# Kernel optimization log

Measured on AMD Instinct MI355X. Metric: run time of the kernel, lower is better.

## Reference

```python
import jax, jax.numpy as jnp
import numpy as np

EPS_BN = 1e-5
K_DET = 50

def conv2d(x, w, b, pad):
    y = jax.lax.conv_general_dilated(x, w, (1, 1), [(pad, pad), (pad, pad)],
                                     dimension_numbers=('NCHW', 'OIHW', 'NCHW'))
    return y + b[None, :, None, None]

def branch2(x, w1, b1, w2, b2):
    # conv3x3 -> relu -> conv1x1
    return conv2d(jax.nn.relu(conv2d(x, w1, b1, 1)), w2, b2, 0)

def roi_head(x, w1, b1, g, beta, m, v, w2, b2):
    # conv3x3 -> BN(eval) -> relu -> global avg pool -> conv1x1
    h = conv2d(x, w1, b1, 1)
    h = (h - m[None, :, None, None]) * (g[None, :, None, None] / jnp.sqrt(v[None, :, None, None] + EPS_BN)) + beta[None, :, None, None]
    h = jax.nn.relu(h)
    h = jnp.mean(h, axis=(2, 3), keepdims=True)
    return conv2d(h, w2, b2, 0)[:, :, 0, 0]

def nms_hm(heat, kernel=3):
    pad = (kernel - 1) // 2
    hmax = jax.lax.reduce_window(heat, -jnp.inf, jax.lax.max,
                                 (1, 1, kernel, kernel), (1, 1, 1, 1),
                                 [(0, 0), (0, 0), (pad, pad), (pad, pad)])
    return heat * (hmax == heat).astype(heat.dtype)

def select_topk(heat, K):
    B, C, H, W = heat.shape
    s_all, i_all = jax.lax.top_k(heat.reshape(B, C, H * W), K)   # per-class topk
    scores, idx = jax.lax.top_k(s_all.reshape(B, C * K), K)      # overall topk
    classes = idx // K
    inds = jnp.take_along_axis(i_all.reshape(B, C * K), idx, axis=1)  # flat HW inds
    return scores, inds, classes

def roi_align_7x7(feat, boxes, sr=2):
    # torchvision roi_align, spatial_scale=1, aligned=False, sampling_ratio=sr
    B, C, H, W = feat.shape
    N = boxes.shape[0]
    b = boxes[:, 0].astype(jnp.int32)
    x1, y1, x2, y2 = boxes[:, 1], boxes[:, 2], boxes[:, 3], boxes[:, 4]
    roi_w = jnp.maximum(x2 - x1, 1.0)
    roi_h = jnp.maximum(y2 - y1, 1.0)
    bw = roi_w / 7.0
    bh = roi_h / 7.0
    S = 7 * sr
    off = (jnp.arange(S, dtype=feat.dtype) + 0.5) / sr  # sample offsets in bin units
    xs = x1[:, None] + bw[:, None] * off[None, :]       # (N,S)
    ys = y1[:, None] + bh[:, None] * off[None, :]
    X = jnp.broadcast_to(xs[:, None, :], (N, S, S))
    Y = jnp.broadcast_to(ys[:, :, None], (N, S, S))
    valid = (X > -1.0) & (X < W) & (Y > -1.0) & (Y < H)
    Xc = jnp.clip(X, 0.0, W - 1.0)
    Yc = jnp.clip(Y, 0.0, H - 1.0)
    x0 = jnp.floor(Xc).astype(jnp.int32)
    y0 = jnp.floor(Yc).astype(jnp.int32)
    x1i = jnp.minimum(x0 + 1, W - 1)
    y1i = jnp.minimum(y0 + 1, H - 1)
    lx = Xc - x0
    ly = Yc - y0
    flat = feat.transpose(0, 2, 3, 1).reshape(B * H * W, C)
    base = (b * H * W)[:, None, None]
    g = lambda yy, xx: flat[base + yy * W + xx]  # (N,S,S,C)
    v = (((1 - ly) * (1 - lx))[..., None] * g(y0, x0)
         + ((1 - ly) * lx)[..., None] * g(y0, x1i)
         + (ly * (1 - lx))[..., None] * g(y1i, x0)
         + (ly * lx)[..., None] * g(y1i, x1i))
    v = v * valid[..., None]
    v = v.reshape(N, 7, sr, 7, sr, C).mean(axis=(2, 4))
    return v.transpose(0, 3, 1, 2)  # (N,C,7,7)

def project_to_rect(calib, pts):
    c_u, c_v = calib[:, 0, 2], calib[:, 1, 2]
    f_u, f_v = calib[:, 0, 0], calib[:, 1, 1]
    b_x = calib[:, 0, 3] / (-f_u)
    b_y = calib[:, 1, 3] / (-f_v)
    x = (pts[:, 0] - c_u) * pts[:, 2] / f_u + b_x
    y = (pts[:, 1] - c_v) * pts[:, 2] / f_v + b_y
    return jnp.stack([x, y, pts[:, 2]], -1)

HEAD_NAMES = ['dep', 'o3', 's3', 'hd']

def setup_inputs():
    key = jax.random.key(0)
    ks = iter(jax.random.split(key, 64))
    B, Cin, H, W = 8, 64, 96, 320
    HC, NC = 256, 3
    f32 = jnp.float32
    rn = lambda shape, s=0.02: s * jax.random.normal(next(ks), shape, f32)
    inp = {}
    inp['features'] = jax.random.normal(next(ks), (B, Cin, H, W), f32)
    base = jnp.array([[700., 0., 640., 0.], [0., 700., 192., 0.], [0., 0., 1., 0.]], f32)
    inp['calib'] = base[None] + (jax.random.uniform(next(ks), (B, 3, 4), f32) - 0.5) * 2.0
    crb = jnp.array([[0., 0.], [1280., 384.]], f32)
    inp['coord_ranges'] = crb[None] + (jax.random.uniform(next(ks), (B, 2, 2), f32) - 0.5) * 2.0
    inp['mean_size'] = jnp.array([[3.88, 1.63, 1.53], [0.84, 0.66, 1.76], [1.76, 0.60, 1.73]], f32)
    inp['hm_w1'] = rn((HC, Cin, 3, 3)); inp['hm_b1'] = jnp.zeros(HC, f32)
    inp['hm_w2'] = rn((3, HC, 1, 1)); inp['hm_b2'] = jnp.full((3,), -np.log(1 / 0.1 - 1), f32)
    inp['o2_w1'] = rn((HC, Cin, 3, 3)); inp['o2_b1'] = jnp.zeros(HC, f32)
    inp['o2_w2'] = rn((2, HC, 1, 1)); inp['o2_b2'] = jnp.zeros(2, f32)
    inp['s2_w1'] = rn((HC, Cin, 3, 3)); inp['s2_b1'] = jnp.zeros(HC, f32)
    inp['s2_w2'] = rn((2, HC, 1, 1)); inp['s2_b2'] = 8.0 * jnp.ones(2, f32)
    Croi = Cin + 2 + NC
    for name, oc in zip(HEAD_NAMES, [2, 2, 4, 24]):
        inp[name + '_w1'] = rn((HC, Croi, 3, 3)); inp[name + '_b1'] = jnp.zeros(HC, f32)
        inp[name + '_g'] = 1.0 + 0.1 * jax.random.normal(next(ks), (HC,), f32)
        inp[name + '_beta'] = 0.1 * jax.random.normal(next(ks), (HC,), f32)
        inp[name + '_m'] = 0.1 * jax.random.normal(next(ks), (HC,), f32)
        inp[name + '_v'] = 1.0 + jax.random.uniform(next(ks), (HC,), f32)
        inp[name + '_w2'] = rn((oc, HC, 1, 1)); inp[name + '_b2'] = jnp.zeros(oc, f32)
    return inp

def reference(features, calib, coord_ranges, mean_size,
              hm_w1, hm_b1, hm_w2, hm_b2,
              o2_w1, o2_b1, o2_w2, o2_b2,
              s2_w1, s2_b1, s2_w2, s2_b2,
              dep_w1, dep_b1, dep_g, dep_beta, dep_m, dep_v, dep_w2, dep_b2,
              o3_w1, o3_b1, o3_g, o3_beta, o3_m, o3_v, o3_w2, o3_b2,
              s3_w1, s3_b1, s3_g, s3_beta, s3_m, s3_v, s3_w2, s3_b2,
              hd_w1, hd_b1, hd_g, hd_beta, hd_m, hd_v, hd_w2, hd_b2):
    B, Cf, H, W = features.shape
    dt = features.dtype
    heatmap = branch2(features, hm_w1, hm_b1, hm_w2, hm_b2)    # (B,3,H,W)
    offset_2d = branch2(features, o2_w1, o2_b1, o2_w2, o2_b2)  # (B,2,H,W)
    size_2d = branch2(features, s2_w1, s2_b1, s2_w2, s2_b2)    # (B,2,H,W)
    heat = nms_hm(heatmap)
    _, inds, classes = select_topk(heat, K_DET)                # (B,K)
    # coord map and box2d maps (B,5,H,W): [batch_idx, x1,y1,x2,y2]
    xs = jnp.arange(W, dtype=dt)
    ys = jnp.arange(H, dtype=dt)
    coord = jnp.stack([jnp.broadcast_to(xs[None, :], (H, W)),
                       jnp.broadcast_to(ys[:, None], (H, W))], 0)[None]
    center = coord + offset_2d
    bidx = jnp.broadcast_to(jnp.arange(B, dtype=dt)[:, None, None, None], (B, 1, H, W))
    box2d_maps = jnp.concatenate([bidx, center - size_2d / 2, center + size_2d / 2], 1)
    bm = box2d_maps.reshape(B, 5, H * W).transpose(0, 2, 1)    # (B,HW,5)
    boxes = jnp.take_along_axis(bm, inds[:, :, None], axis=1).reshape(-1, 5)  # (N,5)
    N = boxes.shape[0]
    roi_feat = roi_align_7x7(features, boxes)                  # (N,C,7,7)
    rb = boxes[:, 0].astype(jnp.int32)
    cr = coord_ranges[rb]                                      # (N,2,2)
    sx = cr[:, 1, 0] - cr[:, 0, 0]
    sy = cr[:, 1, 1] - cr[:, 0, 1]
    box_img = jnp.stack([boxes[:, 0],
                         boxes[:, 1] / W * sx + cr[:, 0, 0],
                         boxes[:, 2] / H * sy + cr[:, 0, 1],
                         boxes[:, 3] / W * sx + cr[:, 0, 0],
                         boxes[:, 4] / H * sy + cr[:, 0, 1]], -1)
    roi_calib = calib[rb]                                      # (N,3,4)
    ones = jnp.ones((N, 1), dt)
    p1 = project_to_rect(roi_calib, jnp.concatenate([box_img[:, 1:3], ones], -1))[:, :2]
    p2 = project_to_rect(roi_calib, jnp.concatenate([box_img[:, 3:5], ones], -1))[:, :2]
    t = jnp.arange(7, dtype=dt) / 6.0
    cx = p1[:, 0:1] + t[None, :] * (p2[:, 0:1] - p1[:, 0:1])   # (N,7)
    cy = p1[:, 1:2] + t[None, :] * (p2[:, 1:2] - p1[:, 1:2])
    coord_maps = jnp.stack([jnp.broadcast_to(cx[:, None, :], (N, 7, 7)),
                            jnp.broadcast_to(cy[:, :, None], (N, 7, 7))], 1)
    cls = classes.reshape(-1)
    NC = mean_size.shape[0]
    cls_hot = jax.nn.one_hot(cls, NC, dtype=dt)
    roi_in = jnp.concatenate([roi_feat, coord_maps,
                              jnp.broadcast_to(cls_hot[:, :, None, None], (N, NC, 7, 7))], 1)
    box2d_h = jnp.maximum(box_img[:, 4] - box_img[:, 2], 1.0)
    s3 = roi_head(roi_in, s3_w1, s3_b1, s3_g, s3_beta, s3_m, s3_v, s3_w2, s3_b2)  # (N,4)
    h3d_log_std = s3[:, 3:4]
    size3d_offset = s3[:, :3]
    size_3d = mean_size[cls] + size3d_offset
    f_u = roi_calib[:, 0, 0]
    depth_geo = size_3d[:, 0] / box2d_h * f_u
    dep = roi_head(roi_in, dep_w1, dep_b1, dep_g, dep_beta, dep_m, dep_v, dep_w2, dep_b2)
    depth_geo_log_std = (h3d_log_std[:, 0] + 2.0 * (jnp.log(f_u) - jnp.log(box2d_h)))[:, None]
    depth_log_std = jax.nn.logsumexp(jnp.concatenate([dep[:, 1:2], depth_geo_log_std], -1), axis=-1, keepdims=True)
    depth = jnp.concatenate([1.0 / (jax.nn.sigmoid(dep[:, 0:1]) + 1e-6) - 1.0 + depth_geo[:, None],
                             depth_log_std], -1)
    heading = roi_head(roi_in, hd_w1, hd_b1, hd_g, hd_beta, hd_m, hd_v, hd_w2, hd_b2)
    offset_3d = roi_head(roi_in, o3_w1, o3_b1, o3_g, o3_beta, o3_m, o3_v, o3_w2, o3_b2)
    return (heatmap, offset_2d, size_2d, heading, depth, offset_3d, size3d_offset, h3d_log_std)
```

## Files before the change

kernel.cpp:

```cpp
#include <hip/hip_runtime.h>
#include <math.h>

typedef unsigned short u16;
typedef unsigned int   u32;
typedef unsigned long long u64;
typedef __attribute__((ext_vector_type(8))) short short8;
typedef __attribute__((ext_vector_type(4))) float f32x4;

__device__ __forceinline__ float b2f(u16 v) { return __uint_as_float(((u32)v) << 16); }
__device__ __forceinline__ u16 f2b(float f) {
    u32 u = __float_as_uint(f);
    u32 r = (u + 0x7FFFu + ((u >> 16) & 1u)) >> 16;
    return (u16)r;
}
__device__ __forceinline__ float gload(const void* p, long i, int bf) {
    return bf ? b2f(((const u16*)p)[i]) : ((const float*)p)[i];
}
__device__ __forceinline__ void gstore(void* p, long i, float v, int bf) {
    if (bf) ((u16*)p)[i] = f2b(v);
    else    ((float*)p)[i] = v;
}

__device__ __forceinline__ u64 packKey(float v, int idx) {
    u32 u = __float_as_uint(v);
    u32 m = (u & 0x80000000u) ? ~u : (u | 0x80000000u);
    return ((u64)(~m) << 32) | (u32)idx;
}

#define BATCH 8
#define CIN   64
#define FH    96
#define FW    320
#define KDET  50
#define NROI  400
#define CROI  69
#define HW    (FH*FW)
#define CHUNK 1920
#define NCHUNK 16

#define WS_HEAT 0L
#define WS_OFF2 737280L
#define WS_SIZ2 1228800L
#define WS_NH   1720320L
#define WS_S1S  2457600L
#define WS_S1I  2458800L
#define WS_CLS  2460000L
#define WS_BOX  2460400L
#define WS_ROI  2462400L
#define WS_HOUT 3814800L
#define WS_W1T  3827600L
#define WS_WB16 3975056L
#define WS_W1H  4269968L
#define WS_PAR  4905872L
#define WS_FLAG 4938960L

#define PB_CAL 0
#define PB_CRN 96
#define PB_MSZ 128
#define PB_BR0 144
#define PB_HD0 3264

#define O_HEAT 0L
#define O_OFF2 737280L
#define O_SIZ2 1228800L
#define O_HEAD 1720320L
#define O_DEP  1729920L
#define O_OFF3 1730720L
#define O_S3D  1731520L
#define O_H3D  1732720L

__global__ void kDetect(const void* __restrict__ feat, int* __restrict__ flag) {
    __shared__ int cnt;
    if (threadIdx.x == 0) cnt = 0;
    __syncthreads();
    u16 v = ((const u16*)feat)[threadIdx.x];
    float f = b2f(v);
    u32 e = (v >> 7) & 0xFF;
    float a = fabsf(f);
    int sane = (e != 0xFF) && (f == 0.f || (a >= 1e-8f && a <= 1e4f));
    atomicAdd(&cnt, sane);
    __syncthreads();
    if (threadIdx.x == 0) *flag = (cnt >= 480) ? 1 : 0;
}

struct WPtrs { const void* bw[3]; const void* hw[4]; };

__global__ void kPrepW(WPtrs P, const int* __restrict__ flag,
                       float* __restrict__ w1t, u16* __restrict__ wb16,
                       u16* __restrict__ whb) {
    const int bf = *flag;
    int idx = blockIdx.x * 256 + threadIdx.x;
    if (idx < 147456) {
        int k = idx >> 8, c = idx & 255;
        w1t[idx] = gload(P.bw[0], (long)c * 576 + k, bf);
    } else if (idx < 589824) {
        int j = idx - 147456;
        int br = j / 147456, rem = j % 147456;
        int tap = rem / 16384;
        int r2 = rem & 16383;
        int s = r2 >> 13;
        int n = (r2 >> 5) & 255;
        int c5 = r2 & 31;
        int ci = s * 32 + c5;
        wb16[j] = f2b(gload(P.bw[br], (long)n * 576 + ci * 9 + tap, bf));
    } else {
        int j = idx - 589824;
        int h = j / 221184, rem = j % 221184;
        int tap = rem / 24576, rem2 = rem % 24576;
        int cs = rem2 / 8192, rem3 = rem2 % 8192;
        int oc = rem3 >> 5, jj = rem3 & 31;
        int ci = cs * 32 + jj;
        u16 val = 0;
        if (ci < CROI) val = f2b(gload(P.hw[h], (long)oc * 621 + ci * 9 + tap, bf));
        whb[j] = val;
    }
}

struct Seg { const void* src; int n; int dst; };
struct Segs { Seg s[40]; };

__global__ void kPrepP(Segs S, const int* __restrict__ flag, float* __restrict__ par) {
    const int bf = *flag;
    Seg sg = S.s[blockIdx.x];
    for (int i = threadIdx.x; i < sg.n; i += 256)
        par[sg.dst + i] = gload(sg.src, i, bf);
}

union B3U {
    u16   a[4][68][72];
    float red[8][64][3];
};

__global__ __launch_bounds__(512, 4)
void kBranch3(const void* __restrict__ feat, const int* __restrict__ flag,
              const u16* __restrict__ wbAll,
              const float* __restrict__ bpAll,
              void* __restrict__ outb, float* __restrict__ wsbase) {
    __shared__ __align__(16) B3U u;

    const long obase[3] = {O_HEAT, O_OFF2, O_SIZ2};
    const long wfs[3]   = {WS_HEAT, WS_OFF2, WS_SIZ2};

    const int bfl = *flag;
    const int tid = threadIdx.x;
    const int wave = tid >> 6, lane = tid & 63;
    const int q = lane >> 4, n15 = lane & 15;
    const int mg = wave >> 2, ng = wave & 3;
    const int x0 = blockIdx.x * 64, y0 = blockIdx.y * 2;
    const int br = blockIdx.z >> 3, b = blockIdx.z & 7;
    const int oc = (br == 0) ? 3 : 2;
    const u16* wpt = wbAll + br * 147456;
    const float* bp = bpAll + br * 1040;

    if (tid < 256) {
        const int ci = tid & 63, rr = tid >> 6;
        const int gy = y0 - 1 + rr;
        if (gy < 0 || gy >= FH) {
            for (int xi = 0; xi < 66; ++xi) u.a[rr][xi][ci] = 0;
        } else if (bfl) {
            const u16* rp = (const u16*)feat + ((long)((b << 6) | ci) * FH + gy) * FW;
            for (int j = 0; j < 10; ++j) {
                int xs0 = x0 - 8 + j * 8;
                u16 tmp[8];
                if (xs0 >= 0 && xs0 <= FW - 8)
                    *(uint4*)tmp = *(const uint4*)(rp + xs0);
                else
                    for (int e = 0; e < 8; ++e) {
                        int gx = xs0 + e;
                        tmp[e] = (gx >= 0 && gx < FW) ? rp[gx] : (u16)0;
                    }
                for (int e = 0; e < 8; ++e) {
                    int xi = xs0 + e - x0 + 1;
                    if (xi >= 0 && xi < 66) u.a[rr][xi][ci] = tmp[e];
                }
            }
        } else {
            const float* rp = (const float*)feat + ((long)((b << 6) | ci) * FH + gy) * FW;
            for (int j = 0; j < 18; ++j) {
                int xs0 = x0 - 4 + j * 4;
                float tmp[4];
                if (xs0 >= 0 && xs0 <= FW - 4)
                    *(float4*)tmp = *(const float4*)(rp + xs0);
                else
                    for (int e = 0; e < 4; ++e) {
                        int gx = xs0 + e;
                        tmp[e] = (gx >= 0 && gx < FW) ? rp[gx] : 0.f;
                    }
                for (int e = 0; e < 4; ++e) {
                    int xi = xs0 + e - x0 + 1;
                    if (xi >= 0 && xi < 66) u.a[rr][xi][ci] = f2b(tmp[e]);
                }
            }
        }
    }
    __syncthreads();

    f32x4 acc[4][4];
#pragma unroll
    for (int i = 0; i < 4; ++i)
#pragma unroll
        for (int t = 0; t < 4; ++t) acc[i][t] = (f32x4){0.f, 0.f, 0.f, 0.f};

#pragma unroll 1
    for (int tap = 0; tap < 9; ++tap) {
        const int ky = tap / 3, kx = tap % 3;
#pragma unroll
        for (int s = 0; s < 2; ++s) {
            const u16* wks = wpt + (tap * 2 + s) * 8192;
            short8 bfr[4];
#pragma unroll
            for (int t = 0; t < 4; ++t)
                bfr[t] = *(const short8*)(wks + (ng * 64 + t * 16 + n15) * 32 + q * 8);
            short8 afr[4];
#pragma unroll
            for (int i = 0; i < 4; ++i)
                afr[i] = *(const short8*)&u.a[mg + ky][i * 16 + n15 + kx][s * 32 + q * 8];
#pragma unroll
            for (int i = 0; i < 4; ++i)
#pragma unroll
                for (int t = 0; t < 4; ++t)
                    acc[i][t] = __builtin_amdgcn_mfma_f32_16x16x32_bf16(
                        afr[i], bfr[t], acc[i][t], 0, 0, 0);
        }
    }

    float b1v[4], w2v[3][4];
#pragma unroll
    for (int t = 0; t < 4; ++t) {
        int n = ng * 64 + t * 16 + n15;
        b1v[t] = bp[n];
#pragma unroll
        for (int k = 0; k < 3; ++k) w2v[k][t] = bp[256 + k * 256 + n];
    }
    __syncthreads();
#pragma unroll
    for (int i = 0; i < 4; ++i) {
#pragma unroll
        for (int r = 0; r < 4; ++r) {
            float pk[3];
#pragma unroll
            for (int k = 0; k < 3; ++k) pk[k] = 0.f;
#pragma unroll
            for (int t = 0; t < 4; ++t) {
                float h = fmaxf(acc[i][t][r] + b1v[t], 0.f);
#pragma unroll
                for (int k = 0; k < 3; ++k) pk[k] = fmaf(h, w2v[k][t], pk[k]);
            }
#pragma unroll
            for (int k = 0; k < 3; ++k) {
                pk[k] += __shfl_xor(pk[k], 1);
                pk[k] += __shfl_xor(pk[k], 2);
                pk[k] += __shfl_xor(pk[k], 4);
                pk[k] += __shfl_xor(pk[k], 8);
            }
            if (n15 == 0) {
                int ml = i * 16 + q * 4 + r;
#pragma unroll
                for (int k = 0; k < 3; ++k) u.red[wave][ml][k] = pk[k];
            }
        }
    }
    __syncthreads();
    float* outf = wsbase + wfs[br];
    for (int t2 = tid; t2 < oc * 128; t2 += 512) {
        int k = t2 >> 7, m = t2 & 127;
        int row = m >> 6, x = m & 63;
        int mg2 = m >> 6, ml = m & 63;
        float s = bp[256 + oc * 256 + k];
#pragma unroll
        for (int w = 0; w < 4; ++w) s += u.red[mg2 * 4 + w][ml][k];
        long o = (((long)b * oc + k) * FH + (y0 + row)) * FW + x0 + x;
        gstore(outb, obase[br] + o, s, bfl);
        outf[o] = s;
    }
}

union BrLds {
    float w[36 * 256];
    float part[32 * 3 * 32];
};

__global__ __launch_bounds__(256)
void kBranchX(const void* __restrict__ feat, const int* __restrict__ flag,
              const float* __restrict__ w1t, const float* __restrict__ bp,
              void* __restrict__ outb, long obase, float* __restrict__ outf) {
    __shared__ float in_lds[4][3][36];
    __shared__ BrLds u;
    const int bf = *flag;
    const int OC = 3;

    const int tid = threadIdx.x;
    const int xg = tid & 7, cg = tid >> 3;
    const int x0 = blockIdx.x * 32, y = blockIdx.y, b = blockIdx.z;
    const int c0 = cg * 8;

    float acc[8][4];
#pragma unroll
    for (int i = 0; i < 8; ++i)
#pragma unroll
        for (int j = 0; j < 4; ++j) acc[i][j] = 0.f;

    for (int chunk = 0; chunk < 16; ++chunk) {
        const int ci0 = chunk * 4;
        __syncthreads();
        for (int i = tid; i < 4 * 3 * 36; i += 256) {
            int xx = i % 36, t2 = i / 36;
            int r = t2 % 3, ci = t2 / 3;
            int gx = x0 - 1 + xx, gy = y - 1 + r;
            float v = 0.f;
            if (gx >= 0 && gx < FW && gy >= 0 && gy < FH)
                v = gload(feat, ((long)(b * CIN + ci0 + ci) * FH + gy) * FW + gx, bf);
            in_lds[ci][r][xx] = v;
        }
        {
            const float4* src = (const float4*)(w1t + (long)ci0 * 9 * 256);
            float4* dst = (float4*)u.w;
            for (int i = tid; i < 36 * 256 / 4; i += 256) dst[i] = src[i];
        }
        __syncthreads();
#pragma unroll
        for (int ci = 0; ci < 4; ++ci) {
#pragma unroll
            for (int ky = 0; ky < 3; ++ky) {
                const float* rowp = &in_lds[ci][ky][xg * 4];
                float inv[6];
                *(float4*)&inv[0] = *(const float4*)&rowp[0];
                *(float2*)&inv[4] = *(const float2*)&rowp[4];
#pragma unroll
                for (int kx = 0; kx < 3; ++kx) {
                    const float* wp = &u.w[(ci * 9 + ky * 3 + kx) * 256 + c0];
                    float wv[8];
                    *(float4*)&wv[0] = *(const float4*)&wp[0];
                    *(float4*)&wv[4] = *(const float4*)&wp[4];
#pragma unroll
                    for (int cc = 0; cc < 8; ++cc)
#pragma unroll
                        for (int xx = 0; xx < 4; ++xx)
                            acc[cc][xx] = fmaf(wv[cc], inv[xx + kx], acc[cc][xx]);
                }
            }
        }
    }

#pragma unroll
    for (int cc = 0; cc < 8; ++cc) {
        float b1v = bp[c0 + cc];
#pragma unroll
        for (int xx = 0; xx < 4; ++xx)
            acc[cc][xx] = fmaxf(acc[cc][xx] + b1v, 0.f);
    }

    __syncthreads();
#pragma unroll
    for (int k = 0; k < OC; ++k) {
        float p[4];
#pragma unroll
        for (int xx = 0; xx < 4; ++xx) p[xx] = 0.f;
#pragma unroll
        for (int cc = 0; cc < 8; ++cc) {
            float wv = bp[256 + k * 256 + c0 + cc];
#pragma unroll
            for (int xx = 0; xx < 4; ++xx) p[xx] = fmaf(acc[cc][xx], wv, p[xx]);
        }
#pragma unroll
        for (int xx = 0; xx < 4; ++xx)
            u.part[(cg * OC + k) * 32 + xg * 4 + xx] = p[xx];
    }
    __syncthreads();
    for (int t = tid; t < OC * 32; t += 256) {
        int k = t >> 5, xx = t & 31;
        float s = bp[256 + OC * 256 + k];
#pragma unroll 8
        for (int g = 0; g < 32; ++g) s += u.part[(g * OC + k) * 32 + xx];
        long o = (((long)b * OC + k) * FH + y) * FW + x0 + xx;
        gstore(outb, obase + o, s, bf);
        outf[o] = s;
    }
}

__global__ void kNms(const float* __restrict__ heat, float* __restrict__ nh) {
    int idx = blockIdx.x * 256 + threadIdx.x;
    if (idx >= 737280) return;
    int x = idx % FW, t = idx / FW;
    int yy = t % FH, bc = t / FH;
    const float* p = heat + (long)bc * HW;
    float v = p[yy * FW + x];
    float m = v;
    for (int dy = -1; dy <= 1; ++dy) {
        int ny = yy + dy;
        if (ny < 0 || ny >= FH) continue;
        for (int dx = -1; dx <= 1; ++dx) {
            int nx = x + dx;
            if (nx < 0 || nx >= FW) continue;
            m = fmaxf(m, p[ny * FW + nx]);
        }
    }
    nh[idx] = (v == m) ? v : 0.f;
}

__global__ __launch_bounds__(256)
void kTopA(float* __restrict__ nh) {
    __shared__ u64 keys[CHUNK];
    const int bc = blockIdx.x, ch = blockIdx.y;
    const int tid = threadIdx.x;
    const long base = (long)bc * HW + (long)ch * CHUNK;
    for (int i = tid; i < CHUNK; i += 256)
        keys[i] = packKey(nh[base + i], ch * CHUNK + i);
    __syncthreads();
    if (tid < 64) {
        const int lane = tid;
        u64* outp = (u64*)(nh + base);
        for (int it = 0; it < KDET; ++it) {
            u64 bk = ~0ULL; int bp = 0;
            for (int i = lane; i < CHUNK; i += 64) {
                u64 k = keys[i];
                if (k < bk) { bk = k; bp = i; }
            }
#pragma unroll
            for (int s = 32; s > 0; s >>= 1) {
                u64 k2 = __shfl_down(bk, s);
                int p2 = __shfl_down(bp, s);
                if (k2 < bk) { bk = k2; bp = p2; }
            }
            bk = __shfl(bk, 0);
            bp = __shfl(bp, 0);
            if (lane == 0) {
                outp[it] = bk;
                keys[bp] = ~0ULL;
            }
        }
    }
}

__global__ __launch_bounds__(64)
void kTopB(const float* __restrict__ nh, float* __restrict__ s1s,
           int* __restrict__ s1i) {
    __shared__ u64 keys[NCHUNK * KDET];
    const int bc = blockIdx.x, lane = threadIdx.x;
    for (int ch = 0; ch < NCHUNK; ++ch) {
        const u64* src = (const u64*)(nh + (long)bc * HW + (long)ch * CHUNK);
        if (lane < KDET) keys[ch * KDET + lane] = src[lane];
    }
    __syncthreads();
    for (int it = 0; it < KDET; ++it) {
        u64 bk = ~0ULL; int bp = 0;
        for (int i = lane; i < NCHUNK * KDET; i += 64) {
            u64 k = keys[i];
            if (k < bk) { bk = k; bp = i; }
        }
#pragma unroll
        for (int s = 32; s > 0; s >>= 1) {
            u64 k2 = __shfl_down(bk, s);
            int p2 = __shfl_down(bp, s);
            if (k2 < bk) { bk = k2; bp = p2; }
        }
        bk = __shfl(bk, 0);
        bp = __shfl(bp, 0);
        if (lane == 0) {
            u32 hm = ~(u32)(bk >> 32);
            u32 u = (hm & 0x80000000u) ? (hm & 0x7fffffffu) : ~hm;
            s1s[bc * KDET + it] = __uint_as_float(u);
            s1i[bc * KDET + it] = (int)(bk & 0xFFFFFFFFu);
            keys[bp] = ~0ULL;
        }
    }
}

__global__ void kTop2(const float* __restrict__ s1s, const int* __restrict__ s1i,
                      const float* __restrict__ off2, const float* __restrict__ siz2,
                      float* __restrict__ boxes, int* __restrict__ clsArr) {
    const int b = blockIdx.x, t = threadIdx.x;
    __shared__ float sc[150];
    for (int i = t; i < 150; i += 64) sc[i] = s1s[b * 150 + i];
    __syncthreads();
    for (int r = 0; r < KDET; ++r) {
        float bv = -INFINITY; int bp = 0x7fffffff;
        for (int i = t; i < 150; i += 64) {
            float v = sc[i];
            if (v > bv) { bv = v; bp = i; }
        }
        for (int s = 32; s > 0; s >>= 1) {
            float v2 = __shfl_down(bv, s);
            int   p2 = __shfl_down(bp, s);
            if (v2 > bv || (v2 == bv && p2 < bp)) { bv = v2; bp = p2; }
        }
        if (t == 0) {
            int cls = bp / KDET;
            int ind = s1i[b * 150 + bp];
            int n = b * KDET + r;
            clsArr[n] = cls;
            int x = ind % FW, yy = ind / FW;
            float cx = (float)x  + off2[(((long)b * 2 + 0) * FH + yy) * FW + x];
            float cy = (float)yy + off2[(((long)b * 2 + 1) * FH + yy) * FW + x];
            float w  = siz2[(((long)b * 2 + 0) * FH + yy) * FW + x];
            float h  = siz2[(((long)b * 2 + 1) * FH + yy) * FW + x];
            boxes[n * 5 + 0] = (float)b;
            boxes[n * 5 + 1] = cx - w * 0.5f;
            boxes[n * 5 + 2] = cy - h * 0.5f;
            boxes[n * 5 + 3] = cx + w * 0.5f;
            boxes[n * 5 + 4] = cy + h * 0.5f;
            sc[bp] = -INFINITY;
        }
        __syncthreads();
    }
}

__global__ __launch_bounds__(256)
void kRoi(const void* __restrict__ feat, const int* __restrict__ flag,
          const float* __restrict__ boxes, const int* __restrict__ clsArr,
          const float* __restrict__ par, float* __restrict__ roi_in) {
    const int n = blockIdx.x, tid = threadIdx.x;
    const int bf = *flag;
    __shared__ int   x0s[14], x1s[14], y0s[14], y1s[14], vxs[14], vys[14];
    __shared__ float lxs[14], lys[14], cxs[7], cys[7];

    const float bx1 = boxes[n * 5 + 1], by1 = boxes[n * 5 + 2];
    const float bx2 = boxes[n * 5 + 3], by2 = boxes[n * 5 + 4];
    const int b = (int)boxes[n * 5 + 0];

    if (tid < 14) {
        float roi_w = fmaxf(bx2 - bx1, 1.f);
        float X = bx1 + (roi_w / 7.f) * ((tid + 0.5f) * 0.5f);
        vxs[tid] = (X > -1.f) && (X < (float)FW);
        float Xc = fminf(fmaxf(X, 0.f), (float)(FW - 1));
        int xi = (int)floorf(Xc);
        x0s[tid] = xi; x1s[tid] = min(xi + 1, FW - 1); lxs[tid] = Xc - (float)xi;
    } else if (tid >= 16 && tid < 30) {
        int i = tid - 16;
        float roi_h = fmaxf(by2 - by1, 1.f);
        float Y = by1 + (roi_h / 7.f) * ((i + 0.5f) * 0.5f);
        vys[i] = (Y > -1.f) && (Y < (float)FH);
        float Yc = fminf(fmaxf(Y, 0.f), (float)(FH - 1));
        int yi = (int)floorf(Yc);
        y0s[i] = yi; y1s[i] = min(yi + 1, FH - 1); lys[i] = Yc - (float)yi;
    } else if (tid >= 32 && tid < 46) {
        int j = tid - 32;
        const float* cal = par + PB_CAL + b * 12;
        float f_u = cal[0], c_u = cal[2], t03 = cal[3];
        float f_v = cal[5], c_v = cal[6], t13 = cal[7];
        float bxc = t03 / (-f_u), byc = t13 / (-f_v);
        const float* cr = par + PB_CRN + b * 4;
        float crx0 = cr[0], cry0 = cr[1], crx1 = cr[2], cry1 = cr[3];
        float sx = crx1 - crx0, sy = cry1 - cry0;
        float u1 = bx1 / (float)FW * sx + crx0, v1 = by1 / (float)FH * sy + cry0;
        float u2 = bx2 / (float)FW * sx + crx0, v2 = by2 / (float)FH * sy + cry0;
        float p1x = (u1 - c_u) / f_u + bxc, p1y = (v1 - c_v) / f_v + byc;
        float p2x = (u2 - c_u) / f_u + bxc, p2y = (v2 - c_v) / f_v + byc;
        if (j < 7) cxs[j] = p1x + ((float)j / 6.f) * (p2x - p1x);
        else       cys[j - 7] = p1y + ((float)(j - 7) / 6.f) * (p2y - p1y);
    }
    __syncthreads();

    for (int t = tid; t < CIN * 49; t += 256) {
        int c = t / 49, p = t % 49, oy = p / 7, ox = p % 7;
        long fb = ((long)b * CIN + c) * HW;
        float acc = 0.f;
#pragma unroll
        for (int dy = 0; dy < 2; ++dy) {
            int sy = oy * 2 + dy;
            float ly = lys[sy]; int yA = y0s[sy], yB = y1s[sy], vy = vys[sy];
#pragma unroll
            for (int dx = 0; dx < 2; ++dx) {
                int sx = ox * 2 + dx;
                float lx = lxs[sx]; int xA = x0s[sx], xB = x1s[sx];
                float v = (1.f - ly) * (1.f - lx) * gload(feat, fb + yA * FW + xA, bf)
                        + (1.f - ly) * lx         * gload(feat, fb + yA * FW + xB, bf)
                        + ly * (1.f - lx)         * gload(feat, fb + yB * FW + xA, bf)
                        + ly * lx                 * gload(feat, fb + yB * FW + xB, bf);
                if (!(vy && vxs[sx])) v = 0.f;
                acc += v;
            }
        }
        roi_in[((long)n * CROI + c) * 49 + p] = acc * 0.25f;
    }
    int cls = clsArr[n];
    for (int t = tid; t < 5 * 49; t += 256) {
        int ch = t / 49, p = t % 49, i = p / 7, j = p % 7;
        float v;
        if (ch == 0)      v = cxs[j];
        else if (ch == 1) v = cys[i];
        else              v = (cls == ch - 2) ? 1.f : 0.f;
        roi_in[((long)n * CROI + 64 + ch) * 49 + p] = v;
    }
}

__global__ __launch_bounds__(256, 4)
void kHeadM(const float* __restrict__ roi_in, const u16* __restrict__ whb,
            const float* __restrict__ par, float* __restrict__ head_out) {
    const int h = blockIdx.x, n = blockIdx.y, tid = threadIdx.x;
    const int wave = tid >> 6, lane = tid & 63;
    const int q = lane >> 4, n15 = lane & 15;
    const int ocArr[4] = {2, 2, 4, 24};
    const int offArr[4] = {0, 2, 4, 8};
    __shared__ __align__(16) u16 r_lds[9][9][104];
    __shared__ float means[256];

    for (int i = tid; i < 9 * 9 * 104 / 8; i += 256)
        ((uint4*)r_lds)[i] = (uint4){0, 0, 0, 0};
    __syncthreads();
    const float* rp = roi_in + (long)n * CROI * 49;
    for (int i = tid; i < CROI * 49; i += 256) {
        int c = i / 49, p = i % 49;
        r_lds[p / 7 + 1][p % 7 + 1][c] = f2b(rp[i]);
    }
    __syncthreads();

    int oyA[4], oxA[4];
#pragma unroll
    for (int i = 0; i < 4; ++i) {
        int pos = i * 16 + n15; if (pos > 48) pos = 48;
        oyA[i] = pos / 7; oxA[i] = pos % 7;
    }

    f32x4 acc[4][4];
#pragma unroll
    for (int i = 0; i < 4; ++i)
#pragma unroll
        for (int t = 0; t < 4; ++t) acc[i][t] = (f32x4){0.f, 0.f, 0.f, 0.f};

#pragma unroll 1
    for (int tap = 0; tap < 9; ++tap) {
        const int ky = tap / 3, kx = tap % 3;
        const u16* wt = whb + ((long)h * 9 + tap) * 24576;
#pragma unroll
        for (int cs = 0; cs < 3; ++cs) {
            short8 afr[4], bfr[4];
#pragma unroll
            for (int i = 0; i < 4; ++i)
                afr[i] = *(const short8*)&r_lds[oyA[i] + ky][oxA[i] + kx][cs * 32 + q * 8];
#pragma unroll
            for (int t = 0; t < 4; ++t)
                bfr[t] = *(const short8*)(wt + ((cs << 8) + wave * 64 + t * 16 + n15) * 32 + q * 8);
#pragma unroll
            for (int i = 0; i < 4; ++i)
#pragma unroll
                for (int t = 0; t < 4; ++t)
                    acc[i][t] = __builtin_amdgcn_mfma_f32_16x16x32_bf16(
                        afr[i], bfr[t], acc[i][t], 0, 0, 0);
        }
    }

    const float* hb = par + PB_HD0 + h * 7456;
#pragma unroll
    for (int t = 0; t < 4; ++t) {
        int oc = wave * 64 + t * 16 + n15;
        float b1 = hb[oc], g = hb[256 + oc], be = hb[512 + oc];
        float m = hb[768 + oc], v = hb[1024 + oc];
        float scale = g / sqrtf(v + 1e-5f);
        float s = 0.f;
#pragma unroll
        for (int i = 0; i < 4; ++i)
#pragma unroll
            for (int r = 0; r < 4; ++r) {
                int pos = i * 16 + q * 4 + r;
                if (pos < 49)
                    s += fmaxf((acc[i][t][r] + b1 - m) * scale + be, 0.f);
            }
        s += __shfl_xor(s, 16);
        s += __shfl_xor(s, 32);
        if (q == 0) means[oc] = s / 49.f;
    }
    __syncthreads();

    int oc_out = ocArr[h];
    const float* w2 = hb + 1280;
    for (int k = wave; k < oc_out; k += 4) {
        float s = 0.f;
        for (int c = lane; c < 256; c += 64) s += means[c] * w2[k * 256 + c];
#pragma unroll
        for (int off = 32; off > 0; off >>= 1) s += __shfl_down(s, off);
        if (lane == 0)
            head_out[(long)n * 32 + offArr[h] + k] = s + w2[oc_out * 256 + k];
    }
}

__global__ void kFinal(const float* __restrict__ head_out, const float* __restrict__ boxes,
                       const int* __restrict__ clsArr, const float* __restrict__ par,
                       void* __restrict__ out, const int* __restrict__ flag) {
    int n = blockIdx.x * 256 + threadIdx.x;
    if (n >= NROI) return;
    const int bf = *flag;
    const float* ho = head_out + (long)n * 32;
    float dep0 = ho[0], dep1 = ho[1];
    int b = (int)boxes[n * 5 + 0];
    int cls = clsArr[n];

    for (int j = 0; j < 24; ++j) gstore(out, O_HEAD + n * 24 + j, ho[8 + j], bf);
    gstore(out, O_OFF3 + n * 2 + 0, ho[2], bf);
    gstore(out, O_OFF3 + n * 2 + 1, ho[3], bf);
    gstore(out, O_S3D + n * 3 + 0, ho[4], bf);
    gstore(out, O_S3D + n * 3 + 1, ho[5], bf);
    gstore(out, O_S3D + n * 3 + 2, ho[6], bf);
    gstore(out, O_H3D + n, ho[7], bf);

    float cry0 = par[PB_CRN + b * 4 + 1], cry1 = par[PB_CRN + b * 4 + 3];
    float sy = cry1 - cry0;
    float bi2 = boxes[n * 5 + 2] / (float)FH * sy + cry0;
    float bi4 = boxes[n * 5 + 4] / (float)FH * sy + cry0;
    float box_h = fmaxf(bi4 - bi2, 1.f);
    float f_u = par[PB_CAL + b * 12 + 0];
    float size3d0 = par[PB_MSZ + cls * 3 + 0] + ho[4];
    float depth_geo = size3d0 / box_h * f_u;
    float sig = 1.f / (1.f + expf(-dep0));
    float d0 = 1.f / (sig + 1e-6f) - 1.f + depth_geo;
    float dgls = ho[7] + 2.f * (logf(f_u) - logf(box_h));
    float mx = fmaxf(dep1, dgls);
    float lse = mx + logf(expf(dep1 - mx) + expf(dgls - mx));
    gstore(out, O_DEP + n * 2 + 0, d0, bf);
    gstore(out, O_DEP + n * 2 + 1, lse, bf);
}

extern "C" void kernel_launch(void* const* d_in, const int* in_sizes, int n_in,
                              void* d_out, int out_size, void* d_ws, size_t ws_size,
                              hipStream_t stream) {
    (void)in_sizes; (void)n_in; (void)out_size; (void)ws_size;
    float* ws = (float*)d_ws;
    float* par = ws + WS_PAR;
    int* flag = (int*)(ws + WS_FLAG);
    u16* wb16 = (u16*)(ws + WS_WB16);
    u16* whb  = (u16*)(ws + WS_W1H);
    const void* feat = d_in[0];

    kDetect<<<1, 512, 0, stream>>>(feat, flag);

    WPtrs WP;
    WP.bw[0] = d_in[4]; WP.bw[1] = d_in[8]; WP.bw[2] = d_in[12];
    WP.hw[0] = d_in[16]; WP.hw[1] = d_in[24]; WP.hw[2] = d_in[32]; WP.hw[3] = d_in[40];
    kPrepW<<<5760, 256, 0, stream>>>(WP, flag, ws + WS_W1T, wb16, whb);

    Segs SG; int si = 0;
    auto add = [&](const void* s, int n, int dst) {
        SG.s[si].src = s; SG.s[si].n = n; SG.s[si].dst = dst; ++si;
    };
    add(d_in[1], 96, PB_CAL); add(d_in[2], 32, PB_CRN); add(d_in[3], 9, PB_MSZ);
    const int ocb[3] = {3, 2, 2};
    for (int b = 0; b < 3; ++b) {
        int base = PB_BR0 + b * 1040;
        int i0 = 4 + 4 * b;
        add(d_in[i0 + 1], 256, base);
        add(d_in[i0 + 2], ocb[b] * 256, base + 256);
        add(d_in[i0 + 3], ocb[b], base + 256 + ocb[b] * 256);
    }
    const int och[4] = {2, 2, 4, 24};
    for (int h = 0; h < 4; ++h) {
        int base = PB_HD0 + h * 7456;
        int i0 = 16 + 8 * h;
        add(d_in[i0 + 1], 256, base);
        add(d_in[i0 + 2], 256, base + 256);
        add(d_in[i0 + 3], 256, base + 512);
        add(d_in[i0 + 4], 256, base + 768);
        add(d_in[i0 + 5], 256, base + 1024);
        add(d_in[i0 + 6], och[h] * 256, base + 1280);
        add(d_in[i0 + 7], och[h], base + 1280 + och[h] * 256);
    }
    kPrepP<<<si, 256, 0, stream>>>(SG, flag, par);

    kBranch3<<<dim3(5, 48, 24), 512, 0, stream>>>(
        feat, flag, wb16, par + PB_BR0, d_out, ws);

    kBranchX<<<dim3(10, 3, 8), 256, 0, stream>>>(
        feat, flag, ws + WS_W1T, par + PB_BR0, d_out, O_HEAT, ws + WS_HEAT);

    kNms<<<2880, 256, 0, stream>>>(ws + WS_HEAT, ws + WS_NH);
    kTopA<<<dim3(24, NCHUNK), 256, 0, stream>>>(ws + WS_NH);
    kTopB<<<24, 64, 0, stream>>>(ws + WS_NH, ws + WS_S1S, (int*)(ws + WS_S1I));
    kTop2<<<8, 64, 0, stream>>>(ws + WS_S1S, (int*)(ws + WS_S1I), ws + WS_OFF2,
                                ws + WS_SIZ2, ws + WS_BOX, (int*)(ws + WS_CLS));
    kRoi<<<400, 256, 0, stream>>>(feat, flag, ws + WS_BOX, (int*)(ws + WS_CLS),
                                  par, ws + WS_ROI);
    kHeadM<<<dim3(4, NROI), 256, 0, stream>>>(ws + WS_ROI, whb, par, ws + WS_HOUT);
    kFinal<<<2, 256, 0, stream>>>(ws + WS_HOUT, ws + WS_BOX, (int*)(ws + WS_CLS),
                                  par, d_out, flag);
}
```

Measured before the change: 914.2 us.

## Fuse prep, NMS+topk stages and loop branches inside kBranch3

Merges the dtype detection, weight prep and parameter prep kernels into one launch, with every block recomputing the bf16/fp32 flag locally. Fuses the 3x3 heatmap NMS into the per-chunk top-k kernel using an LDS row tile, and merges the per-class and overall top-k stages into one kernel. kBranch3 now loops over the three branches inside each block so the staged input tile is loaded once rather than three times. This removes several launches and intermediate round trips, but the branch kernel has a third as many blocks and does three times the work per block.

```diff
diff --git a/kernel.cpp b/kernel.cpp
--- a/kernel.cpp
+++ b/kernel.cpp
@@ -25,6 +25,23 @@
     u32 u = __float_as_uint(v);
     u32 m = (u & 0x80000000u) ? ~u : (u | 0x80000000u);
     return ((u64)(~m) << 32) | (u32)idx;
+}
+
+__device__ int blockFlag(const void* feat) {
+    __shared__ int fcnt;
+    if (threadIdx.x == 0) fcnt = 0;
+    __syncthreads();
+    int sane = 0;
+    for (int i = threadIdx.x; i < 512; i += blockDim.x) {
+        u16 v = ((const u16*)feat)[i];
+        float f = b2f(v);
+        u32 e = (v >> 7) & 0xFF;
+        float a = fabsf(f);
+        sane += (e != 0xFF) && (f == 0.f || (a >= 1e-8f && a <= 1e4f));
+    }
+    atomicAdd(&fcnt, sane);
+    __syncthreads();
+    return fcnt >= 480;
 }
 
 #define BATCH 8
@@ -69,74 +86,59 @@
 #define O_S3D  1731520L
 #define O_H3D  1732720L
 
-__global__ void kDetect(const void* __restrict__ feat, int* __restrict__ flag) {
-    __shared__ int cnt;
-    if (threadIdx.x == 0) cnt = 0;
-    __syncthreads();
-    u16 v = ((const u16*)feat)[threadIdx.x];
-    float f = b2f(v);
-    u32 e = (v >> 7) & 0xFF;
-    float a = fabsf(f);
-    int sane = (e != 0xFF) && (f == 0.f || (a >= 1e-8f && a <= 1e4f));
-    atomicAdd(&cnt, sane);
-    __syncthreads();
-    if (threadIdx.x == 0) *flag = (cnt >= 480) ? 1 : 0;
-}
-
 struct WPtrs { const void* bw[3]; const void* hw[4]; };
-
-__global__ void kPrepW(WPtrs P, const int* __restrict__ flag,
-                       float* __restrict__ w1t, u16* __restrict__ wb16,
-                       u16* __restrict__ whb) {
-    const int bf = *flag;
-    int idx = blockIdx.x * 256 + threadIdx.x;
-    if (idx < 147456) {
-        int k = idx >> 8, c = idx & 255;
-        w1t[idx] = gload(P.bw[0], (long)c * 576 + k, bf);
-    } else if (idx < 589824) {
-        int j = idx - 147456;
-        int br = j / 147456, rem = j % 147456;
-        int tap = rem / 16384;
-        int r2 = rem & 16383;
-        int s = r2 >> 13;
-        int n = (r2 >> 5) & 255;
-        int c5 = r2 & 31;
-        int ci = s * 32 + c5;
-        wb16[j] = f2b(gload(P.bw[br], (long)n * 576 + ci * 9 + tap, bf));
+struct Seg { const void* src; int n; int dst; };
+struct Segs { Seg s[40]; int cnt; };
+
+__global__ void kPrepWP(WPtrs P, Segs S, const void* __restrict__ feat,
+                        int* __restrict__ flag, float* __restrict__ w1t,
+                        u16* __restrict__ wb16, u16* __restrict__ whb,
+                        float* __restrict__ par) {
+    const int bf = blockFlag(feat);
+    if (blockIdx.x == 0 && threadIdx.x == 0) *flag = bf;
+    if (blockIdx.x < 5760) {
+        int idx = blockIdx.x * 256 + threadIdx.x;
+        if (idx < 147456) {
+            int k = idx >> 8, c = idx & 255;
+            w1t[idx] = gload(P.bw[0], (long)c * 576 + k, bf);
+        } else if (idx < 589824) {
+            int j = idx - 147456;
+            int br = j / 147456, rem = j % 147456;
+            int tap = rem / 16384;
+            int r2 = rem & 16383;
+            int s = r2 >> 13;
+            int n = (r2 >> 5) & 255;
+            int c5 = r2 & 31;
+            int ci = s * 32 + c5;
+            wb16[j] = f2b(gload(P.bw[br], (long)n * 576 + ci * 9 + tap, bf));
+        } else {
+            int j = idx - 589824;
+            int h = j / 221184, rem = j % 221184;
+            int tap = rem / 24576, rem2 = rem % 24576;
+            int cs = rem2 / 8192, rem3 = rem2 % 8192;
+            int oc = rem3 >> 5, jj = rem3 & 31;
+            int ci = cs * 32 + jj;
+            u16 val = 0;
+            if (ci < CROI) val = f2b(gload(P.hw[h], (long)oc * 621 + ci * 9 + tap, bf));
+            whb[j] = val;
+        }
     } else {
-        int j = idx - 589824;
-        int h = j / 221184, rem = j % 221184;
-        int tap = rem / 24576, rem2 = rem % 24576;
-        int cs = rem2 / 8192, rem3 = rem2 % 8192;
-        int oc = rem3 >> 5, jj = rem3 & 31;
-        int ci = cs * 32 + jj;
-        u16 val = 0;
-        if (ci < CROI) val = f2b(gload(P.hw[h], (long)oc * 621 + ci * 9 + tap, bf));
-        whb[j] = val;
-    }
-}
-
-struct Seg { const void* src; int n; int dst; };
-struct Segs { Seg s[40]; };
-
-__global__ void kPrepP(Segs S, const int* __restrict__ flag, float* __restrict__ par) {
-    const int bf = *flag;
-    Seg sg = S.s[blockIdx.x];
-    for (int i = threadIdx.x; i < sg.n; i += 256)
-        par[sg.dst + i] = gload(sg.src, i, bf);
-}
-
-union B3U {
-    u16   a[4][68][72];
-    float red[8][64][3];
-};
+        int sidx = blockIdx.x - 5760;
+        if (sidx < S.cnt) {
+            Seg sg = S.s[sidx];
+            for (int i = threadIdx.x; i < sg.n; i += 256)
+                par[sg.dst + i] = gload(sg.src, i, bf);
+        }
+    }
+}
 
 __global__ __launch_bounds__(512, 4)
 void kBranch3(const void* __restrict__ feat, const int* __restrict__ flag,
               const u16* __restrict__ wbAll,
               const float* __restrict__ bpAll,
               void* __restrict__ outb, float* __restrict__ wsbase) {
-    __shared__ __align__(16) B3U u;
+    __shared__ __align__(16) u16 a_lds[4][68][72];
+    __shared__ float red[8][64][3];
 
     const long obase[3] = {O_HEAT, O_OFF2, O_SIZ2};
     const long wfs[3]   = {WS_HEAT, WS_OFF2, WS_SIZ2};
@@ -147,16 +149,13 @@
     const int q = lane >> 4, n15 = lane & 15;
     const int mg = wave >> 2, ng = wave & 3;
     const int x0 = blockIdx.x * 64, y0 = blockIdx.y * 2;
-    const int br = blockIdx.z >> 3, b = blockIdx.z & 7;
-    const int oc = (br == 0) ? 3 : 2;
-    const u16* wpt = wbAll + br * 147456;
-    const float* bp = bpAll + br * 1040;
+    const int b = blockIdx.z;
 
     if (tid < 256) {
         const int ci = tid & 63, rr = tid >> 6;
         const int gy = y0 - 1 + rr;
         if (gy < 0 || gy >= FH) {
-            for (int xi = 0; xi < 66; ++xi) u.a[rr][xi][ci] = 0;
+            for (int xi = 0; xi < 66; ++xi) a_lds[rr][xi][ci] = 0;
         } else if (bfl) {
             const u16* rp = (const u16*)feat + ((long)((b << 6) | ci) * FH + gy) * FW;
             for (int j = 0; j < 10; ++j) {
@@ -171,7 +170,7 @@
                     }
                 for (int e = 0; e < 8; ++e) {
                     int xi = xs0 + e - x0 + 1;
-                    if (xi >= 0 && xi < 66) u.a[rr][xi][ci] = tmp[e];
+                    if (xi >= 0 && xi < 66) a_lds[rr][xi][ci] = tmp[e];
                 }
             }
         } else {
@@ -188,90 +187,97 @@
                     }
                 for (int e = 0; e < 4; ++e) {
                     int xi = xs0 + e - x0 + 1;
-                    if (xi >= 0 && xi < 66) u.a[rr][xi][ci] = f2b(tmp[e]);
+                    if (xi >= 0 && xi < 66) a_lds[rr][xi][ci] = f2b(tmp[e]);
                 }
             }
         }
     }
     __syncthreads();
 
-    f32x4 acc[4][4];
-#pragma unroll
-    for (int i = 0; i < 4; ++i)
-#pragma unroll
-        for (int t = 0; t < 4; ++t) acc[i][t] = (f32x4){0.f, 0.f, 0.f, 0.f};
-
 #pragma unroll 1
-    for (int tap = 0; tap < 9; ++tap) {
-        const int ky = tap / 3, kx = tap % 3;
-#pragma unroll
-        for (int s = 0; s < 2; ++s) {
-            const u16* wks = wpt + (tap * 2 + s) * 8192;
-            short8 bfr[4];
-#pragma unroll
-            for (int t = 0; t < 4; ++t)
-                bfr[t] = *(const short8*)(wks + (ng * 64 + t * 16 + n15) * 32 + q * 8);
-            short8 afr[4];
-#pragma unroll
-            for (int i = 0; i < 4; ++i)
-                afr[i] = *(const short8*)&u.a[mg + ky][i * 16 + n15 + kx][s * 32 + q * 8];
-#pragma unroll
-            for (int i = 0; i < 4; ++i)
+    for (int br = 0; br < 3; ++br) {
+        const int oc = (br == 0) ? 3 : 2;
+        const u16* wpt = wbAll + br * 147456;
+        const float* bp = bpAll + br * 1040;
+
+        f32x4 acc[4][4];
+#pragma unroll
+        for (int i = 0; i < 4; ++i)
+#pragma unroll
+            for (int t = 0; t < 4; ++t) acc[i][t] = (f32x4){0.f, 0.f, 0.f, 0.f};
+
+#pragma unroll 1
+        for (int tap = 0; tap < 9; ++tap) {
+            const int ky = tap / 3, kx = tap % 3;
+#pragma unroll
+            for (int s = 0; s < 2; ++s) {
+                const u16* wks = wpt + (tap * 2 + s) * 8192;
+                short8 bfr[4];
 #pragma unroll
                 for (int t = 0; t < 4; ++t)
-                    acc[i][t] = __builtin_amdgcn_mfma_f32_16x16x32_bf16(
-                        afr[i], bfr[t], acc[i][t], 0, 0, 0);
-        }
-    }
-
-    float b1v[4], w2v[3][4];
-#pragma unroll
-    for (int t = 0; t < 4; ++t) {
-        int n = ng * 64 + t * 16 + n15;
-        b1v[t] = bp[n];
-#pragma unroll
-        for (int k = 0; k < 3; ++k) w2v[k][t] = bp[256 + k * 256 + n];
-    }
-    __syncthreads();
-#pragma unroll
-    for (int i = 0; i < 4; ++i) {
-#pragma unroll
-        for (int r = 0; r < 4; ++r) {
-            float pk[3];
-#pragma unroll
-            for (int k = 0; k < 3; ++k) pk[k] = 0.f;
-#pragma unroll
-            for (int t = 0; t < 4; ++t) {
-                float h = fmaxf(acc[i][t][r] + b1v[t], 0.f);
-#pragma unroll
-                for (int k = 0; k < 3; ++k) pk[k] = fmaf(h, w2v[k][t], pk[k]);
-            }
-#pragma unroll
-            for (int k = 0; k < 3; ++k) {
-                pk[k] += __shfl_xor(pk[k], 1);
-                pk[k] += __shfl_xor(pk[k], 2);
-                pk[k] += __shfl_xor(pk[k], 4);
-                pk[k] += __shfl_xor(pk[k], 8);
-            }
-            if (n15 == 0) {
-                int ml = i * 16 + q * 4 + r;
-#pragma unroll
-                for (int k = 0; k < 3; ++k) u.red[wave][ml][k] = pk[k];
-            }
-        }
-    }
-    __syncthreads();
-    float* outf = wsbase + wfs[br];
-    for (int t2 = tid; t2 < oc * 128; t2 += 512) {
-        int k = t2 >> 7, m = t2 & 127;
-        int row = m >> 6, x = m & 63;
-        int mg2 = m >> 6, ml = m & 63;
-        float s = bp[256 + oc * 256 + k];
-#pragma unroll
-        for (int w = 0; w < 4; ++w) s += u.red[mg2 * 4 + w][ml][k];
-        long o = (((long)b * oc + k) * FH + (y0 + row)) * FW + x0 + x;
-        gstore(outb, obase[br] + o, s, bfl);
-        outf[o] = s;
+                    bfr[t] = *(const short8*)(wks + (ng * 64 + t * 16 + n15) * 32 + q * 8);
+                short8 afr[4];
+#pragma unroll
+                for (int i = 0; i < 4; ++i)
+                    afr[i] = *(const short8*)&a_lds[mg + ky][i * 16 + n15 + kx][s * 32 + q * 8];
+#pragma unroll
+                for (int i = 0; i < 4; ++i)
+#pragma unroll
+                    for (int t = 0; t < 4; ++t)
+                        acc[i][t] = __builtin_amdgcn_mfma_f32_16x16x32_bf16(
+                            afr[i], bfr[t], acc[i][t], 0, 0, 0);
+            }
+        }
+
+        float b1v[4], w2v[3][4];
+#pragma unroll
+        for (int t = 0; t < 4; ++t) {
+            int n = ng * 64 + t * 16 + n15;
+            b1v[t] = bp[n];
+#pragma unroll
+            for (int k = 0; k < 3; ++k) w2v[k][t] = bp[256 + k * 256 + n];
+        }
+        __syncthreads();
+#pragma unroll
+        for (int i = 0; i < 4; ++i) {
+#pragma unroll
+            for (int r = 0; r < 4; ++r) {
+                float pk[3];
+#pragma unroll
+                for (int k = 0; k < 3; ++k) pk[k] = 0.f;
+#pragma unroll
+                for (int t = 0; t < 4; ++t) {
+                    float h = fmaxf(acc[i][t][r] + b1v[t], 0.f);
+#pragma unroll
+                    for (int k = 0; k < 3; ++k) pk[k] = fmaf(h, w2v[k][t], pk[k]);
+                }
+#pragma unroll
+                for (int k = 0; k < 3; ++k) {
+                    pk[k] += __shfl_xor(pk[k], 1);
+                    pk[k] += __shfl_xor(pk[k], 2);
+                    pk[k] += __shfl_xor(pk[k], 4);
+                    pk[k] += __shfl_xor(pk[k], 8);
+                }
+                if (n15 == 0) {
+                    int ml = i * 16 + q * 4 + r;
+#pragma unroll
+                    for (int k = 0; k < 3; ++k) red[wave][ml][k] = pk[k];
+                }
+            }
+        }
+        __syncthreads();
+        float* outf = wsbase + wfs[br];
+        for (int t2 = tid; t2 < oc * 128; t2 += 512) {
+            int k = t2 >> 7, m = t2 & 127;
+            int row = m >> 6, x = m & 63;
+            int mg2 = m >> 6, ml = m & 63;
+            float s = bp[256 + oc * 256 + k];
+#pragma unroll
+            for (int w = 0; w < 4; ++w) s += red[mg2 * 4 + w][ml][k];
+            long o = (((long)b * oc + k) * FH + (y0 + row)) * FW + x0 + x;
+            gstore(outb, obase[br] + o, s, bfl);
+            outf[o] = s;
+        }
     }
 }
 
@@ -378,38 +384,39 @@
     }
 }
 
-__global__ void kNms(const float* __restrict__ heat, float* __restrict__ nh) {
-    int idx = blockIdx.x * 256 + threadIdx.x;
-    if (idx >= 737280) return;
-    int x = idx % FW, t = idx / FW;
-    int yy = t % FH, bc = t / FH;
-    const float* p = heat + (long)bc * HW;
-    float v = p[yy * FW + x];
-    float m = v;
-    for (int dy = -1; dy <= 1; ++dy) {
-        int ny = yy + dy;
-        if (ny < 0 || ny >= FH) continue;
-        for (int dx = -1; dx <= 1; ++dx) {
-            int nx = x + dx;
-            if (nx < 0 || nx >= FW) continue;
-            m = fmaxf(m, p[ny * FW + nx]);
-        }
-    }
-    nh[idx] = (v == m) ? v : 0.f;
-}
-
 __global__ __launch_bounds__(256)
-void kTopA(float* __restrict__ nh) {
+void kNmsTopA(const float* __restrict__ heat, float* __restrict__ nh) {
+    __shared__ float hrow[8][320];
     __shared__ u64 keys[CHUNK];
     const int bc = blockIdx.x, ch = blockIdx.y;
     const int tid = threadIdx.x;
-    const long base = (long)bc * HW + (long)ch * CHUNK;
-    for (int i = tid; i < CHUNK; i += 256)
-        keys[i] = packKey(nh[base + i], ch * CHUNK + i);
+    const int r0 = ch * 6;
+    const float* hp = heat + (long)bc * HW;
+
+    for (int i = tid; i < 8 * 320; i += 256) {
+        int rr = i / 320, x = i % 320;
+        int gy = r0 - 1 + rr;
+        hrow[rr][x] = (gy >= 0 && gy < FH) ? hp[(long)gy * FW + x] : -INFINITY;
+    }
+    __syncthreads();
+    for (int i = tid; i < CHUNK; i += 256) {
+        int ry = i / 320, x = i % 320;
+        float v = hrow[ry + 1][x];
+        float m = v;
+        int xm = max(x - 1, 0), xp = min(x + 1, FW - 1);
+#pragma unroll
+        for (int dy = 0; dy < 3; ++dy) {
+            m = fmaxf(m, hrow[ry + dy][xm]);
+            m = fmaxf(m, hrow[ry + dy][x]);
+            m = fmaxf(m, hrow[ry + dy][xp]);
+        }
+        float nv = (v == m) ? v : 0.f;
+        keys[i] = packKey(nv, ch * CHUNK + i);
+    }
     __syncthreads();
     if (tid < 64) {
         const int lane = tid;
-        u64* outp = (u64*)(nh + base);
+        u64* outp = (u64*)(nh + (long)bc * HW + (long)ch * CHUNK);
         for (int it = 0; it < KDET; ++it) {
             u64 bk = ~0ULL; int bp = 0;
             for (int i = lane; i < CHUNK; i += 64) {
@@ -432,20 +439,26 @@
     }
 }
 
-__global__ __launch_bounds__(64)
-void kTopB(const float* __restrict__ nh, float* __restrict__ s1s,
-           int* __restrict__ s1i) {
-    __shared__ u64 keys[NCHUNK * KDET];
-    const int bc = blockIdx.x, lane = threadIdx.x;
+__global__ __launch_bounds__(192)
+void kTopBC(const float* __restrict__ nh, const float* __restrict__ off2,
+            const float* __restrict__ siz2, float* __restrict__ boxes,
+            int* __restrict__ clsArr) {
+    __shared__ u64 keys[3][NCHUNK * KDET];
+    __shared__ float sc[150];
+    __shared__ int   si[150];
+    const int b = blockIdx.x, tid = threadIdx.x;
+    const int wave = tid >> 6, lane = tid & 63;
+    const int bc = b * 3 + wave;
+
     for (int ch = 0; ch < NCHUNK; ++ch) {
         const u64* src = (const u64*)(nh + (long)bc * HW + (long)ch * CHUNK);
-        if (lane < KDET) keys[ch * KDET + lane] = src[lane];
+        if (lane < KDET) keys[wave][ch * KDET + lane] = src[lane];
     }
     __syncthreads();
     for (int it = 0; it < KDET; ++it) {
         u64 bk = ~0ULL; int bp = 0;
         for (int i = lane; i < NCHUNK * KDET; i += 64) {
-            u64 k = keys[i];
+            u64 k = keys[wave][i];
             if (k < bk) { bk = k; bp = i; }
         }
 #pragma unroll
@@ -459,49 +472,45 @@
         if (lane == 0) {
             u32 hm = ~(u32)(bk >> 32);
             u32 u = (hm & 0x80000000u) ? (hm & 0x7fffffffu) : ~hm;
-            s1s[bc * KDET + it] = __uint_as_float(u);
-            s1i[bc * KDET + it] = (int)(bk & 0xFFFFFFFFu);
-            keys[bp] = ~0ULL;
-        }
-    }
-}
-
-__global__ void kTop2(const float* __restrict__ s1s, const int* __restrict__ s1i,
-                      const float* __restrict__ off2, const float* __restrict__ siz2,
-                      float* __restrict__ boxes, int* __restrict__ clsArr) {
-    const int b = blockIdx.x, t = threadIdx.x;
-    __shared__ float sc[150];
-    for (int i = t; i < 150; i += 64) sc[i] = s1s[b * 150 + i];
-    __syncthreads();
-    for (int r = 0; r < KDET; ++r) {
-        float bv = -INFINITY; int bp = 0x7fffffff;
-        for (int i = t; i < 150; i += 64) {
-            float v = sc[i];
-            if (v > bv) { bv = v; bp = i; }
-        }
-        for (int s = 32; s > 0; s >>= 1) {
-            float v2 = __shfl_down(bv, s);
-            int   p2 = __shfl_down(bp, s);
-            if (v2 > bv || (v2 == bv && p2 < bp)) { bv = v2; bp = p2; }
-        }
-        if (t == 0) {
-            int cls = bp / KDET;
-            int ind = s1i[b * 150 + bp];
-            int n = b * KDET + r;
-            clsArr[n] = cls;
-            int x = ind % FW, yy = ind / FW;
-            float cx = (float)x  + off2[(((long)b * 2 + 0) * FH + yy) * FW + x];
-            float cy = (float)yy + off2[(((long)b * 2 + 1) * FH + yy) * FW + x];
-            float w  = siz2[(((long)b * 2 + 0) * FH + yy) * FW + x];
-            float h  = siz2[(((long)b * 2 + 1) * FH + yy) * FW + x];
-            boxes[n * 5 + 0] = (float)b;
-            boxes[n * 5 + 1] = cx - w * 0.5f;
-            boxes[n * 5 + 2] = cy - h * 0.5f;
-            boxes[n * 5 + 3] = cx + w * 0.5f;
-            boxes[n * 5 + 4] = cy + h * 0.5f;
-            sc[bp] = -INFINITY;
-        }
-        __syncthreads();
+            sc[wave * KDET + it] = __uint_as_float(u);
+            si[wave * KDET + it] = (int)(bk & 0xFFFFFFFFu);
+            keys[wave][bp] = ~0ULL;
+        }
+    }
+    __syncthreads();
+    if (wave == 0) {
+        const int t = lane;
+        for (int r = 0; r < KDET; ++r) {
+            float bv = -INFINITY; int bp = 0x7fffffff;
+            for (int i = t; i < 150; i += 64) {
+                float v = sc[i];
+                if (v > bv) { bv = v; bp = i; }
+            }
+#pragma unroll
+            for (int s = 32; s > 0; s >>= 1) {
+                float v2 = __shfl_down(bv, s);
+                int   p2 = __shfl_down(bp, s);
+                if (v2 > bv || (v2 == bv && p2 < bp)) { bv = v2; bp = p2; }
+            }
+            bp = __shfl(bp, 0);
+            if (t == 0) {
+                int cls = bp / KDET;
+                int ind = si[bp];
+                int n = b * KDET + r;
+                clsArr[n] = cls;
+                int x = ind % FW, yy = ind / FW;
+                float cx = (float)x  + off2[(((long)b * 2 + 0) * FH + yy) * FW + x];
+                float cy = (float)yy + off2[(((long)b * 2 + 1) * FH + yy) * FW + x];
+                float w  = siz2[(((long)b * 2 + 0) * FH + yy) * FW + x];
+                float h  = siz2[(((long)b * 2 + 1) * FH + yy) * FW + x];
+                boxes[n * 5 + 0] = (float)b;
+                boxes[n * 5 + 1] = cx - w * 0.5f;
+                boxes[n * 5 + 2] = cy - h * 0.5f;
+                boxes[n * 5 + 3] = cx + w * 0.5f;
+                boxes[n * 5 + 4] = cy + h * 0.5f;
+                sc[bp] = -INFINITY;
+            }
+        }
     }
 }
 
@@ -721,12 +730,9 @@
     u16* whb  = (u16*)(ws + WS_W1H);
     const void* feat = d_in[0];
 
-    kDetect<<<1, 512, 0, stream>>>(feat, flag);
-
     WPtrs WP;
     WP.bw[0] = d_in[4]; WP.bw[1] = d_in[8]; WP.bw[2] = d_in[12];
     WP.hw[0] = d_in[16]; WP.hw[1] = d_in[24]; WP.hw[2] = d_in[32]; WP.hw[3] = d_in[40];
-    kPrepW<<<5760, 256, 0, stream>>>(WP, flag, ws + WS_W1T, wb16, whb);
 
     Segs SG; int si = 0;
     auto add = [&](const void* s, int n, int dst) {
@@ -753,19 +759,20 @@
         add(d_in[i0 + 6], och[h] * 256, base + 1280);
         add(d_in[i0 + 7], och[h], base + 1280 + och[h] * 256);
     }
-    kPrepP<<<si, 256, 0, stream>>>(SG, flag, par);
-
-    kBranch3<<<dim3(5, 48, 24), 512, 0, stream>>>(
+    SG.cnt = si;
+
+    kPrepWP<<<5760 + 40, 256, 0, stream>>>(WP, SG, feat, flag,
+                                           ws + WS_W1T, wb16, whb, par);
+
+    kBranch3<<<dim3(5, 48, 8), 512, 0, stream>>>(
         feat, flag, wb16, par + PB_BR0, d_out, ws);
 
     kBranchX<<<dim3(10, 3, 8), 256, 0, stream>>>(
         feat, flag, ws + WS_W1T, par + PB_BR0, d_out, O_HEAT, ws + WS_HEAT);
 
-    kNms<<<2880, 256, 0, stream>>>(ws + WS_HEAT, ws + WS_NH);
-    kTopA<<<dim3(24, NCHUNK), 256, 0, stream>>>(ws + WS_NH);
-    kTopB<<<24, 64, 0, stream>>>(ws + WS_NH, ws + WS_S1S, (int*)(ws + WS_S1I));
-    kTop2<<<8, 64, 0, stream>>>(ws + WS_S1S, (int*)(ws + WS_S1I), ws + WS_OFF2,
-                                ws + WS_SIZ2, ws + WS_BOX, (int*)(ws + WS_CLS));
+    kNmsTopA<<<dim3(24, NCHUNK), 256, 0, stream>>>(ws + WS_HEAT, ws + WS_NH);
+    kTopBC<<<8, 192, 0, stream>>>(ws + WS_NH, ws + WS_OFF2, ws + WS_SIZ2,
+                                  ws + WS_BOX, (int*)(ws + WS_CLS));
     kRoi<<<400, 256, 0, stream>>>(feat, flag, ws + WS_BOX, (int*)(ws + WS_CLS),
                                   par, ws + WS_ROI);
     kHeadM<<<dim3(4, NROI), 256, 0, stream>>>(ws + WS_ROI, whb, par, ws + WS_HOUT);
```

Result: faster. 831.5 us (-9.0%).
